# Optimization experiments

Hardware: AMD Instinct MI355X
Metric: run time of the kernel (lower is better)

The kernel has to match this reference:

```python
import jax, jax.numpy as jnp
import numpy as np

B, N_IN, N_OUT = 4096, 64, 64
M = N_IN * N_OUT


def setup_inputs() -> dict:
    key = jax.random.key(0)
    k1, k2, k3, k4 = jax.random.split(key, 4)
    I = jax.random.normal(k1, (B, N_IN, 4, 4), dtype=jnp.float32)
    # params: (rand - 0.5) * 1, matching torch init
    aW = (jax.random.uniform(k2, (M, 1, 1), dtype=jnp.float32) - 0.5)
    uW = (jax.random.uniform(k3, (M, 1, 3), dtype=jnp.float32) - 0.5)
    tW = (jax.random.uniform(k4, (M, 1, 3), dtype=jnp.float32) - 0.5)
    return {"I": I, "aW": aW, "uW": uW, "tW": tW}


def _build_WM(aW, uW, tW, n_in, n_out):
    m = aW.shape[0]
    a = aW.reshape(m, 1, 1)                       # angle per transform
    u = jax.nn.sigmoid(uW.reshape(m, 3))
    u = u / jnp.linalg.norm(u, axis=1, keepdims=True)  # unit axis
    ux, uy, uz = u[:, 0], u[:, 1], u[:, 2]
    z = jnp.zeros_like(ux)
    # skew-symmetric cross-product matrix K
    K = jnp.stack([z, -uz, uy,
                   uz, z, -ux,
                   -uy, ux, z], axis=1).reshape(m, 3, 3)
    uuT = u[:, :, None] * u[:, None, :]
    I3 = jnp.eye(3, dtype=aW.dtype)
    # Rodrigues: R = sin(a) K + cos(a)(I - uu^T) + uu^T
    rot = jnp.sin(a) * K + jnp.cos(a) * (I3 - uuT) + uuT
    top = jnp.concatenate([rot, tW.reshape(m, 3, 1)], axis=2)   # [m,3,4]
    bot = jnp.broadcast_to(jnp.array([[0.0, 0.0, 0.0, 1.0]], dtype=aW.dtype), (m, 1, 4))
    WM = jnp.concatenate([top, bot], axis=1)                    # [m,4,4]
    return WM.reshape(n_in, n_out, 4, 4)


def reference(I, aW, uW, tW):
    batch, n_in = I.shape[0], I.shape[1]
    n_out = aW.shape[0] // n_in
    WM = _build_WM(aW, uW, tW, n_in, n_out)       # [n_in, n_out, 4, 4] (batch-invariant)
    # A[b,j,k] = I[b,j] @ WM[j,k]
    A = jnp.einsum('bjxy,jkyz->jbkxz', I, WM)     # [n_in, B, n_out, 4, 4]
    init = jnp.broadcast_to(jnp.eye(4, dtype=I.dtype), (batch, n_out, 4, 4))
    def step(carry, Aj):
        return jnp.einsum('bkxy,bkyz->bkxz', carry, Aj), None
    O, _ = jax.lax.scan(step, init, A)            # sequential product over n_in
    return O                                      # [B, n_out, 4, 4]
```

## Files before the change

### kernel.cpp

```cpp
#include <hip/hip_runtime.h>

#define BATCH 4096
#define NIN   64
#define NOUT  64
#define M_TOT (NIN * NOUT)

__global__ __launch_bounds__(256) void build_wm_kernel(
    const float* __restrict__ aW, const float* __restrict__ uW,
    const float* __restrict__ tW, float4* __restrict__ WT) {
  int m = blockIdx.x * 256 + threadIdx.x;
  if (m >= M_TOT) return;
  int j = m >> 6, k = m & 63;

  float a  = aW[m];
  float ux = 1.f / (1.f + expf(-uW[3 * m + 0]));
  float uy = 1.f / (1.f + expf(-uW[3 * m + 1]));
  float uz = 1.f / (1.f + expf(-uW[3 * m + 2]));
  float inv = 1.f / sqrtf(ux * ux + uy * uy + uz * uz);
  ux *= inv; uy *= inv; uz *= inv;

  float sa = sinf(a), ca = cosf(a);
  float xx = ux * ux, yy = uy * uy, zz = uz * uz;
  float xy = ux * uy, xz = ux * uz, yz = uy * uz;

  float R00 = ca * (1.f - xx) + xx;
  float R01 = -sa * uz + ca * (-xy) + xy;
  float R02 =  sa * uy + ca * (-xz) + xz;
  float R10 =  sa * uz + ca * (-xy) + xy;
  float R11 = ca * (1.f - yy) + yy;
  float R12 = -sa * ux + ca * (-yz) + yz;
  float R20 = -sa * uy + ca * (-xz) + xz;
  float R21 =  sa * ux + ca * (-yz) + yz;
  float R22 = ca * (1.f - zz) + zz;

  float t0 = tW[3 * m + 0], t1 = tW[3 * m + 1], t2 = tW[3 * m + 2];

  WT[(j * 3 + 0) * 64 + k] = make_float4(R00, R01, R02, t0);
  WT[(j * 3 + 1) * 64 + k] = make_float4(R10, R11, R12, t1);
  WT[(j * 3 + 2) * 64 + k] = make_float4(R20, R21, R22, t2);
}


#define IMUL_TO(D0, D1, D2, D3, r, W0, W1, W2)                       \
  D0 = r.x * W0.x + r.y * W1.x + r.z * W2.x;                         \
  D1 = r.x * W0.y + r.y * W1.y + r.z * W2.y;                         \
  D2 = r.x * W0.z + r.y * W1.z + r.z * W2.z;                         \
  D3 = r.x * W0.w + r.y * W1.w + r.z * W2.w + r.w;

#define CMUL_ROW(x)                                                            \
  {                                                                            \
    float t0 = c[x*4+0]*A00 + c[x*4+1]*A10 + c[x*4+2]*A20 + c[x*4+3]*A30;      \
    float t1 = c[x*4+0]*A01 + c[x*4+1]*A11 + c[x*4+2]*A21 + c[x*4+3]*A31;      \
    float t2 = c[x*4+0]*A02 + c[x*4+1]*A12 + c[x*4+2]*A22 + c[x*4+3]*A32;      \
    float t3 = c[x*4+0]*A03 + c[x*4+1]*A13 + c[x*4+2]*A23 + c[x*4+3]*A33;      \
    c[x*4+0] = t0; c[x*4+1] = t1; c[x*4+2] = t2; c[x*4+3] = t3;                \
  }

#define STEP_FOLD(JJ)                                                          \
  {                                                                            \
    float4 w0 = Wb[(JJ) * 192], w1 = Wb[(JJ) * 192 + 64],                      \
           w2 = Wb[(JJ) * 192 + 128];                                          \
    float4 r0 = Ib[(JJ) * 4 + 0], r1 = Ib[(JJ) * 4 + 1];                       \
    float4 r2 = Ib[(JJ) * 4 + 2], r3 = Ib[(JJ) * 4 + 3];                       \
    float A00, A01, A02, A03, A10, A11, A12, A13;                              \
    float A20, A21, A22, A23, A30, A31, A32, A33;                              \
    IMUL_TO(A00, A01, A02, A03, r0, w0, w1, w2)                                \
    IMUL_TO(A10, A11, A12, A13, r1, w0, w1, w2)                                \
    IMUL_TO(A20, A21, A22, A23, r2, w0, w1, w2)                                \
    IMUL_TO(A30, A31, A32, A33, r3, w0, w1, w2)                                \
    CMUL_ROW(0) CMUL_ROW(1) CMUL_ROW(2) CMUL_ROW(3)                            \
  }

#define LDS_FOLD(q)                                                            \
  {                                                                            \
    float A00 = P[q][lane][0],  A01 = P[q][lane][1];                           \
    float A02 = P[q][lane][2],  A03 = P[q][lane][3];                           \
    float A10 = P[q][lane][4],  A11 = P[q][lane][5];                           \
    float A12 = P[q][lane][6],  A13 = P[q][lane][7];                           \
    float A20 = P[q][lane][8],  A21 = P[q][lane][9];                           \
    float A22 = P[q][lane][10], A23 = P[q][lane][11];                          \
    float A30 = P[q][lane][12], A31 = P[q][lane][13];                          \
    float A32 = P[q][lane][14], A33 = P[q][lane][15];                          \
    CMUL_ROW(0) CMUL_ROW(1) CMUL_ROW(2) CMUL_ROW(3)                            \
  }

__global__ __launch_bounds__(256) void chain_kernel(
    const float4* __restrict__ I4, const float4* __restrict__ WT,
    float4* __restrict__ O4) {
  const int lane = threadIdx.x & 63;
  const int wq   = threadIdx.x >> 6;
  const int b    = (int)blockIdx.x;

  const int ioff = __builtin_amdgcn_readfirstlane((b * NIN + wq * 16) * 4);
  const float4* __restrict__ Ib = I4 + ioff;
  const float4* __restrict__ Wb = WT + (size_t)(wq * 16 * 3) * 64 + lane;

  float c[16];
  {
    float4 w0 = Wb[0], w1 = Wb[64], w2 = Wb[128];
    float4 r0 = Ib[0], r1 = Ib[1], r2 = Ib[2], r3 = Ib[3];
    IMUL_TO(c[0],  c[1],  c[2],  c[3],  r0, w0, w1, w2)
    IMUL_TO(c[4],  c[5],  c[6],  c[7],  r1, w0, w1, w2)
    IMUL_TO(c[8],  c[9],  c[10], c[11], r2, w0, w1, w2)
    IMUL_TO(c[12], c[13], c[14], c[15], r3, w0, w1, w2)
  }

#pragma unroll 5
  for (int j = 1; j < 16; ++j) {
    STEP_FOLD(j)
  }

  __shared__ float P[4][64][17];
  if (wq != 0) {
#pragma unroll
    for (int i = 0; i < 16; i++) P[wq][lane][i] = c[i];
  }
  __syncthreads();
  if (wq == 0) {
    LDS_FOLD(1)
    LDS_FOLD(2)
    LDS_FOLD(3)

    float4* o = O4 + ((size_t)b * NOUT + lane) * 4;
    o[0] = make_float4(c[0],  c[1],  c[2],  c[3]);
    o[1] = make_float4(c[4],  c[5],  c[6],  c[7]);
    o[2] = make_float4(c[8],  c[9],  c[10], c[11]);
    o[3] = make_float4(c[12], c[13], c[14], c[15]);
  }
}

extern "C" void kernel_launch(void* const* d_in, const int* in_sizes, int n_in,
                              void* d_out, int out_size, void* d_ws, size_t ws_size,
                              hipStream_t stream) {
  const float* I  = (const float*)d_in[0];
  const float* aW = (const float*)d_in[1];
  const float* uW = (const float*)d_in[2];
  const float* tW = (const float*)d_in[3];

  float4* WT = (float4*)d_ws;

  build_wm_kernel<<<M_TOT / 256, 256, 0, stream>>>(aW, uW, tW, WT);
  chain_kernel<<<BATCH, 256, 0, stream>>>((const float4*)I, WT, (float4*)d_out);
}
```

Before: 62.76 us.

## Load I rows once per wave and broadcast via readlane; tree-reduce partial products

Each wave now loads its 16x4 float4 rows of I with one coalesced vector load (one float4 per lane) and broadcasts them to all lanes with readlane, replacing uniform scalar/global loads inside the loop. The j-loop is fully unrolled. The cross-wave combine becomes a two-level tree (waves 0 and 2 fold in parallel, then wave 0 folds the result), which shortens the serial tail at the cost of a second barrier. Readlane adds many SALU/VALU moves and higher register pressure from full unrolling.

```diff
diff --git a/kernel.cpp b/kernel.cpp
--- a/kernel.cpp
+++ b/kernel.cpp
@@ -41,11 +41,7 @@
 }
 
 
-#define IMUL_TO(D0, D1, D2, D3, r, W0, W1, W2)                       \
-  D0 = r.x * W0.x + r.y * W1.x + r.z * W2.x;                         \
-  D1 = r.x * W0.y + r.y * W1.y + r.z * W2.y;                         \
-  D2 = r.x * W0.z + r.y * W1.z + r.z * W2.z;                         \
-  D3 = r.x * W0.w + r.y * W1.w + r.z * W2.w + r.w;
+#define RLF(v, L) __int_as_float(__builtin_amdgcn_readlane(__float_as_int(v), (L)))
 
 #define CMUL_ROW(x)                                                            \
   {                                                                            \
@@ -54,21 +50,6 @@
     float t2 = c[x*4+0]*A02 + c[x*4+1]*A12 + c[x*4+2]*A22 + c[x*4+3]*A32;      \
     float t3 = c[x*4+0]*A03 + c[x*4+1]*A13 + c[x*4+2]*A23 + c[x*4+3]*A33;      \
     c[x*4+0] = t0; c[x*4+1] = t1; c[x*4+2] = t2; c[x*4+3] = t3;                \
-  }
-
-#define STEP_FOLD(JJ)                                                          \
-  {                                                                            \
-    float4 w0 = Wb[(JJ) * 192], w1 = Wb[(JJ) * 192 + 64],                      \
-           w2 = Wb[(JJ) * 192 + 128];                                          \
-    float4 r0 = Ib[(JJ) * 4 + 0], r1 = Ib[(JJ) * 4 + 1];                       \
-    float4 r2 = Ib[(JJ) * 4 + 2], r3 = Ib[(JJ) * 4 + 3];                       \
-    float A00, A01, A02, A03, A10, A11, A12, A13;                              \
-    float A20, A21, A22, A23, A30, A31, A32, A33;                              \
-    IMUL_TO(A00, A01, A02, A03, r0, w0, w1, w2)                                \
-    IMUL_TO(A10, A11, A12, A13, r1, w0, w1, w2)                                \
-    IMUL_TO(A20, A21, A22, A23, r2, w0, w1, w2)                                \
-    IMUL_TO(A30, A31, A32, A33, r3, w0, w1, w2)                                \
-    CMUL_ROW(0) CMUL_ROW(1) CMUL_ROW(2) CMUL_ROW(3)                            \
   }
 
 #define LDS_FOLD(q)                                                            \
@@ -91,35 +72,70 @@
   const int wq   = threadIdx.x >> 6;
   const int b    = (int)blockIdx.x;
 
-  const int ioff = __builtin_amdgcn_readfirstlane((b * NIN + wq * 16) * 4);
-  const float4* __restrict__ Ib = I4 + ioff;
+  const float4 myI = I4[(size_t)(b * NIN + wq * 16) * 4 + lane];
   const float4* __restrict__ Wb = WT + (size_t)(wq * 16 * 3) * 64 + lane;
 
   float c[16];
-  {
-    float4 w0 = Wb[0], w1 = Wb[64], w2 = Wb[128];
-    float4 r0 = Ib[0], r1 = Ib[1], r2 = Ib[2], r3 = Ib[3];
-    IMUL_TO(c[0],  c[1],  c[2],  c[3],  r0, w0, w1, w2)
-    IMUL_TO(c[4],  c[5],  c[6],  c[7],  r1, w0, w1, w2)
-    IMUL_TO(c[8],  c[9],  c[10], c[11], r2, w0, w1, w2)
-    IMUL_TO(c[12], c[13], c[14], c[15], r3, w0, w1, w2)
+
+#pragma unroll
+  for (int j = 0; j < 16; ++j) {
+    float4 w0 = Wb[j * 192], w1 = Wb[j * 192 + 64], w2 = Wb[j * 192 + 128];
+
+    float r0x = RLF(myI.x, 4*j+0), r0y = RLF(myI.y, 4*j+0),
+          r0z = RLF(myI.z, 4*j+0), r0w = RLF(myI.w, 4*j+0);
+    float r1x = RLF(myI.x, 4*j+1), r1y = RLF(myI.y, 4*j+1),
+          r1z = RLF(myI.z, 4*j+1), r1w = RLF(myI.w, 4*j+1);
+    float r2x = RLF(myI.x, 4*j+2), r2y = RLF(myI.y, 4*j+2),
+          r2z = RLF(myI.z, 4*j+2), r2w = RLF(myI.w, 4*j+2);
+    float r3x = RLF(myI.x, 4*j+3), r3y = RLF(myI.y, 4*j+3),
+          r3z = RLF(myI.z, 4*j+3), r3w = RLF(myI.w, 4*j+3);
+
+    float A00 = r0x*w0.x + r0y*w1.x + r0z*w2.x;
+    float A01 = r0x*w0.y + r0y*w1.y + r0z*w2.y;
+    float A02 = r0x*w0.z + r0y*w1.z + r0z*w2.z;
+    float A03 = r0x*w0.w + r0y*w1.w + r0z*w2.w + r0w;
+    float A10 = r1x*w0.x + r1y*w1.x + r1z*w2.x;
+    float A11 = r1x*w0.y + r1y*w1.y + r1z*w2.y;
+    float A12 = r1x*w0.z + r1y*w1.z + r1z*w2.z;
+    float A13 = r1x*w0.w + r1y*w1.w + r1z*w2.w + r1w;
+    float A20 = r2x*w0.x + r2y*w1.x + r2z*w2.x;
+    float A21 = r2x*w0.y + r2y*w1.y + r2z*w2.y;
+    float A22 = r2x*w0.z + r2y*w1.z + r2z*w2.z;
+    float A23 = r2x*w0.w + r2y*w1.w + r2z*w2.w + r2w;
+    float A30 = r3x*w0.x + r3y*w1.x + r3z*w2.x;
+    float A31 = r3x*w0.y + r3y*w1.y + r3z*w2.y;
+    float A32 = r3x*w0.z + r3y*w1.z + r3z*w2.z;
+    float A33 = r3x*w0.w + r3y*w1.w + r3z*w2.w + r3w;
+
+    if (j == 0) {
+      c[0]=A00;  c[1]=A01;  c[2]=A02;  c[3]=A03;
+      c[4]=A10;  c[5]=A11;  c[6]=A12;  c[7]=A13;
+      c[8]=A20;  c[9]=A21;  c[10]=A22; c[11]=A23;
+      c[12]=A30; c[13]=A31; c[14]=A32; c[15]=A33;
+    } else {
+      CMUL_ROW(0) CMUL_ROW(1) CMUL_ROW(2) CMUL_ROW(3)
+    }
   }
 
-#pragma unroll 5
-  for (int j = 1; j < 16; ++j) {
-    STEP_FOLD(j)
+  __shared__ float P[3][64][17];
+  if (wq == 1) {
+#pragma unroll
+    for (int i = 0; i < 16; i++) P[0][lane][i] = c[i];
   }
-
-  __shared__ float P[4][64][17];
-  if (wq != 0) {
+  if (wq == 3) {
 #pragma unroll
-    for (int i = 0; i < 16; i++) P[wq][lane][i] = c[i];
+    for (int i = 0; i < 16; i++) P[1][lane][i] = c[i];
+  }
+  __syncthreads();
+  if (wq == 0) { LDS_FOLD(0) }
+  if (wq == 2) {
+    LDS_FOLD(1)
+#pragma unroll
+    for (int i = 0; i < 16; i++) P[2][lane][i] = c[i];
   }
   __syncthreads();
   if (wq == 0) {
-    LDS_FOLD(1)
     LDS_FOLD(2)
-    LDS_FOLD(3)
 
     float4* o = O4 + ((size_t)b * NOUT + lane) * 4;
     o[0] = make_float4(c[0],  c[1],  c[2],  c[3]);
```

Result: slower. 105.1 us (+67.4%).
